# Kernel tuning notes

Hardware: AMD Instinct MI355X
Metric: run time of the kernel (lower is better)

## Reference

```python
import jax, jax.numpy as jnp
import numpy as np

H = 128        # hidden_dim
R = 50         # num_rbf
L = 4          # num_layers
CUTOFF = 5.0
N = 10000      # atoms
M = 64         # molecules
BOX = 54.7     # box side -> ~32 neighbors within cutoff
EPS = 1e-5     # LayerNorm eps (torch default)


def setup_inputs() -> dict:
    rng = np.random.default_rng(0)
    positions = rng.uniform(0.0, BOX, size=(N, 3)).astype(np.float32)
    # static radius graph (the torch module filters a dense NxN pair list by cutoff;
    # we do that once here so runtime shapes are fixed / jit-friendly)
    sq = (positions ** 2).sum(-1)
    d2 = sq[:, None] + sq[None, :] - 2.0 * positions @ positions.T
    mask = (d2 < CUTOFF * CUTOFF) & ~np.eye(N, dtype=bool)
    row, col = np.nonzero(mask)
    edge_index = jnp.asarray(np.stack([row, col]).astype(np.int32))  # [2, E]

    key = jax.random.key(0)
    ks = jax.random.split(key, 6)
    s = 0.05
    return dict(
        atomic_numbers=jax.random.randint(ks[0], (N,), 0, 100),
        positions=jnp.asarray(positions),
        batch=jnp.asarray((np.arange(N) * M // N).astype(np.int32)),  # sorted, all M present
        edge_index=edge_index,
        embedding=jax.random.normal(ks[1], (100, H), jnp.float32) * s,
        W1=jax.random.normal(ks[2], (L, H + R, H), jnp.float32) * s,
        b1=jnp.zeros((L, H), jnp.float32),
        W2=jax.random.normal(ks[3], (L, H, H), jnp.float32) * s,
        b2=jnp.zeros((L, H), jnp.float32),
        W_ih=jax.random.normal(ks[4], (L, H, 3 * H), jnp.float32) * s,
        b_ih=jax.random.normal(ks[5], (L, 3 * H), jnp.float32) * s,
        b_hh=jnp.zeros((L, 3 * H), jnp.float32),
        ln_g=jnp.ones((H,), jnp.float32),
        ln_b=jnp.zeros((H,), jnp.float32),
    )


def reference(atomic_numbers, positions, batch, edge_index, embedding,
              W1, b1, W2, b2, W_ih, b_ih, b_hh, ln_g, ln_b):
    x = embedding[jnp.clip(atomic_numbers, 0, 99)]                  # [N, H]
    row, col = edge_index[0], edge_index[1]
    d = jnp.linalg.norm(positions[row] - positions[col], axis=-1)   # [E]
    centers = jnp.linspace(0.0, CUTOFF, R)
    width = CUTOFF / R
    rbf = jnp.exp(-((d[:, None] - centers) ** 2) / (2.0 * width * width))  # [E, R]
    n_atoms = x.shape[0]
    for l in range(L):
        x_j = x[row]                                                # gather [E, H]
        inp = jnp.concatenate([x_j, rbf], axis=-1)                  # [E, H+R]
        msg = jax.nn.silu(inp @ W1[l] + b1[l]) @ W2[l] + b2[l]      # [E, H]
        aggr = jax.ops.segment_sum(msg, col, num_segments=n_atoms)  # [N, H]
        # GRU step with h0 = 0: W_hh @ h vanishes, only b_hh survives
        gi = aggr @ W_ih[l] + b_ih[l]                               # [N, 3H]
        gi_r, gi_z, gi_n = jnp.split(gi, 3, axis=-1)
        bh_r, bh_z, bh_n = jnp.split(b_hh[l], 3)
        r = jax.nn.sigmoid(gi_r + bh_r)
        z = jax.nn.sigmoid(gi_z + bh_z)
        n = jnp.tanh(gi_n + r * bh_n)
        x = x + (1.0 - z) * n                                       # h' = (1-z)*n + z*0
    mu = x.mean(-1, keepdims=True)
    var = ((x - mu) ** 2).mean(-1, keepdims=True)
    x = (x - mu) / jnp.sqrt(var + EPS) * ln_g + ln_b
    sums = jax.ops.segment_sum(x, batch, num_segments=M)            # [M, H]
    counts = jax.ops.segment_sum(jnp.ones((x.shape[0],), jnp.float32), batch, num_segments=M)
    graph_rep = sums / jnp.clip(counts, 1.0)[:, None]
    return x, graph_rep
```

## Files before the change

kernel.cpp:

```cpp
#include <hip/hip_runtime.h>
#include <hip/hip_bf16.h>
#include <math.h>


#define HH 128
#define RR 50
#define LL 4
#define GA 16
#define L2E 1.4426950408889634f

typedef __attribute__((ext_vector_type(8))) short short8;
typedef __attribute__((ext_vector_type(4))) float floatx4;

__device__ __forceinline__ unsigned short f2bf(float f) {
    unsigned u = __float_as_uint(f);
    unsigned r = (u + 0x7fffu + ((u >> 16) & 1u)) >> 16;
    return (unsigned short)r;
}
__device__ __forceinline__ unsigned pack_bf2(float lo, float hi) {
    unsigned u0 = __float_as_uint(lo) + 0x8000u;
    unsigned u1 = __float_as_uint(hi) + 0x8000u;
    return __builtin_amdgcn_perm(u1, u0, 0x07060302);
}
__device__ __forceinline__ float fast_sigmoid(float x) {
    return __builtin_amdgcn_rcpf(1.f + __builtin_amdgcn_exp2f(x * (-L2E)));
}
__device__ __forceinline__ float fast_tanh(float x) {
    x = fminf(fmaxf(x, -15.f), 15.f);
    float t = __builtin_amdgcn_exp2f(x * (2.f * L2E));
    return (t - 1.f) * __builtin_amdgcn_rcpf(t + 1.f);
}
__device__ __forceinline__ int imin(int a, int b) { return a < b ? a : b; }

__global__ __launch_bounds__(256) void prep_kernel(
    const int* __restrict__ an, const float* __restrict__ emb,
    float* __restrict__ X,
    const float* __restrict__ pos, const int* __restrict__ erow,
    const int* __restrict__ ecol, float* __restrict__ dist,
    int* __restrict__ rowptr, int* __restrict__ bptr,
    const int* __restrict__ batch,
    const float* __restrict__ W1, unsigned short* __restrict__ W1rT,
    unsigned short* __restrict__ W1xT,
    const float* __restrict__ W2, const float* __restrict__ Wih,
    unsigned short* __restrict__ WcT,
    const float* __restrict__ b2, float* __restrict__ P,
    const float* __restrict__ b1, unsigned short* __restrict__ embWbf,
    int* __restrict__ zc, float* __restrict__ outg,
    int N, int E, int M)
{
    int gidx = blockIdx.x * 256 + threadIdx.x;
    int c0 = N * HH;
    if (gidx < c0) {
        int i = gidx >> 7, n = gidx & 127;
        int z = an[i];
        z = z < 0 ? 0 : (z > 99 ? 99 : z);
        X[gidx] = emb[z * HH + n];
        return;
    }
    gidx -= c0;
    int PT = E > N ? E : N;
    if (gidx < PT) {
        int i = gidx;
        if (i < E) {
            int rc = erow[i];
            int rp = (i > 0) ? erow[i - 1] : -1;
            for (int r = rp + 1; r <= rc; ++r) rowptr[r] = i;
            if (i == E - 1)
                for (int r = rc + 1; r <= N; ++r) rowptr[r] = E;
        }
        if (i < N) {
            int bc = batch[i];
            int bp = (i > 0) ? batch[i - 1] : -1;
            for (int m = bp + 1; m <= bc; ++m) bptr[m] = i;
            if (i == N - 1)
                for (int m = bc + 1; m <= M; ++m) bptr[m] = N;
        }
        return;
    }
    gidx -= PT;
    if (gidx < E) {
        int e = gidx;
        int r = erow[e], c = ecol[e];
        float dx = pos[r * 3 + 0] - pos[c * 3 + 0];
        float dy = pos[r * 3 + 1] - pos[c * 3 + 1];
        float dz = pos[r * 3 + 2] - pos[c * 3 + 2];
        dist[e] = sqrtf(dx * dx + dy * dy + dz * dz);
        return;
    }
    gidx -= E;
    if (gidx < LL * HH * 64) {
        int l = gidx >> 13, rem = gidx & 8191;
        int f = rem >> 9, lane2 = (rem >> 3) & 63, j = rem & 7;
        int nt = f >> 1, h = f & 1;
        int n = nt * 16 + (lane2 & 15);
        int k = h * 32 + (lane2 >> 4) * 8 + j;
        float v = (k < RR) ? W1[((size_t)l * 178 + 128 + k) * HH + n] : 0.f;
        W1rT[gidx] = f2bf(v);
        return;
    }
    gidx -= LL * HH * 64;
    if (gidx < LL * HH * HH) {
        int l = gidx >> 14, rem = gidx & 16383, n = rem >> 7, k = rem & 127;
        W1xT[gidx] = f2bf(W1[((size_t)l * 178 + k) * HH + n]);
        return;
    }
    gidx -= LL * HH * HH;
    if (gidx < LL * HH * 384) {
        int l = gidx / (HH * 384), rem = gidx % (HH * 384);
        int i = rem / 384, j = rem % 384;
        const float* w2row = W2 + ((size_t)l * HH + i) * HH;
        const float* wih = Wih + (size_t)l * HH * 384;
        float acc = 0.f;
#pragma unroll 4
        for (int k = 0; k < HH; ++k)
            acc = fmaf(w2row[k], wih[(size_t)k * 384 + j], acc);
        WcT[((size_t)l * 384 + j) * HH + i] = f2bf(acc);
        return;
    }
    gidx -= LL * HH * 384;
    if (gidx < LL * 384) {
        int l = gidx / 384, j = gidx % 384;
        const float* b2l = b2 + (size_t)l * HH;
        const float* wih = Wih + (size_t)l * HH * 384;
        float acc = 0.f;
#pragma unroll 4
        for (int k = 0; k < HH; ++k)
            acc = fmaf(b2l[k], wih[(size_t)k * 384 + j], acc);
        P[gidx] = acc;
        return;
    }
    gidx -= LL * 384;
    if (gidx < N) {
        int z = an[gidx];
        zc[gidx] = z < 0 ? 0 : (z > 99 ? 99 : z);
        return;
    }
    gidx -= N;
    if (gidx < 100 * HH) {
        int z = gidx >> 7, n = gidx & 127;
        const float* er = emb + (size_t)z * HH;
        float acc = b1[n];
#pragma unroll 4
        for (int k = 0; k < HH; ++k)
            acc = fmaf(er[k], W1[(size_t)k * HH + n], acc);
        embWbf[gidx] = f2bf(acc);
        return;
    }
    gidx -= 100 * HH;
    if (gidx < M * HH) {
        outg[gidx] = 0.f;
    }
}

__global__ __launch_bounds__(256) void layer_kernel(
    const unsigned short* __restrict__ Xsrc, const unsigned short* __restrict__ W1rTf,
    const float* __restrict__ dist, const int* __restrict__ rowptr,
    const int* __restrict__ ecol, const int* __restrict__ zc, int use_z,
    const unsigned short* __restrict__ WcT, const float* __restrict__ P,
    const float* __restrict__ bih, const float* __restrict__ bhh,
    float* __restrict__ X, int N,
    const unsigned short* __restrict__ W1xT, const float* __restrict__ b1next,
    unsigned short* __restrict__ XWout, int do_xw,
    int do_ln, const float* __restrict__ lng, const float* __restrict__ lnb,
    const int* __restrict__ batch, const int* __restrict__ bptr,
    float* __restrict__ outx, float* __restrict__ outg)
{
    __shared__ __align__(16) unsigned short W1s[8192];
    __shared__ __align__(16) union ShMem {
        struct { unsigned short Sb[GA][136]; unsigned short Xb[GA][136]; } s;
        struct { float Xf[GA][132]; float pool[2][HH]; } f;
    } sh;
    unsigned short (&Sb)[GA][136] = sh.s.Sb;
    unsigned short (&Xb)[GA][136] = sh.s.Xb;
    float (&Xf)[GA][132] = sh.f.Xf;
    float (&pool)[2][HH] = sh.f.pool;

    int tid = threadIdx.x;
    {
        const uint4* src = (const uint4*)W1rTf;
        uint4* dst = (uint4*)W1s;
#pragma unroll
        for (int i = 0; i < 4; ++i) dst[tid + i * 256] = src[tid + i * 256];
    }
    __syncthreads();

    int abase = blockIdx.x * GA;
    int wavei = tid >> 6, lane = tid & 63;
    int c = lane & 15, q = lane >> 4;

    const float stepc = 5.0f / 49.0f;
    const float negc = -50.f * L2E;
    float kqs = (float)(q << 3) * stepc;

#pragma unroll 1
    for (int uu = wavei; uu < 2 * GA; uu += 4) {
        int a_loc = uu >> 1, h = uu & 1;
        int a = abase + a_loc;
        int es = 0, ee = 0;
        if (a < N) { es = rowptr[a]; ee = rowptr[a + 1]; }
        float acc[4][4];
#pragma unroll
        for (int t = 0; t < 4; ++t)
#pragma unroll
            for (int r = 0; r < 4; ++r) acc[t][r] = 0.f;

        if (es < ee) {
            int last = ee - 1;
            int ce0 = imin(es + c, last);
            float dcur = dist[ce0];
            int c0raw = ecol[ce0];
            int rowcur = use_z ? zc[c0raw] : c0raw;
            int ce1 = imin(es + 16 + c, last);
            float dnxt = dist[ce1];
            int colnxt = ecol[ce1];

            for (int eb = es; eb < ee; eb += 16) {
                const unsigned short* xwrow = Xsrc + (size_t)rowcur * HH + h * 64;
                uint2 gx[4];
#pragma unroll
                for (int t = 0; t < 4; ++t)
                    gx[t] = *(const uint2*)&xwrow[t * 16 + (q << 2)];

                float d_t = dcur;
                dcur = dnxt;
                int rownxt = use_z ? zc[colnxt] : colnxt;
                int ce2 = imin(eb + 32 + c, last);
                dnxt = dist[ce2];
                colnxt = ecol[ce2];
                rowcur = rownxt;

                float dq0 = d_t - kqs;
                float dq1 = dq0 - 32.f * stepc;
                union { unsigned u[4]; short8 s; } ub0, ub1;
#pragma unroll
                for (int p = 0; p < 4; ++p) {
                    float t0 = dq0 - (float)(2 * p) * stepc;
                    float t1 = dq0 - (float)(2 * p + 1) * stepc;
                    float e0f = __builtin_amdgcn_exp2f(negc * t0 * t0);
                    float e1f = __builtin_amdgcn_exp2f(negc * t1 * t1);
                    ub0.u[p] = pack_bf2(e0f, e1f);
                    float t2 = dq1 - (float)(2 * p) * stepc;
                    float t3 = dq1 - (float)(2 * p + 1) * stepc;
                    float e2f = __builtin_amdgcn_exp2f(negc * t2 * t2);
                    float e3f = __builtin_amdgcn_exp2f(negc * t3 * t3);
                    ub1.u[p] = pack_bf2(e2f, e3f);
                }
                short8 B0 = ub0.s, B1 = ub1.s;
                float msk = ((eb + c) < ee) ? 1.f : 0.f;

                unsigned wbyte = (unsigned)(lane * 16);
                asm volatile("" : "+v"(wbyte));
                const char* Wlp = (const char*)W1s + wbyte;

#pragma unroll
                for (int t = 0; t < 4; ++t) {
                    int f0 = (h * 4 + t) * 2;
                    short8 A0 = *(const short8*)(Wlp + f0 * 1024);
                    short8 A1 = *(const short8*)(Wlp + (f0 + 1) * 1024);
                    floatx4 C;
                    C[0] = __uint_as_float(gx[t].x << 16);
                    C[1] = __uint_as_float(gx[t].x & 0xffff0000u);
                    C[2] = __uint_as_float(gx[t].y << 16);
                    C[3] = __uint_as_float(gx[t].y & 0xffff0000u);
                    C = __builtin_amdgcn_mfma_f32_16x16x32_bf16(A0, B0, C, 0, 0, 0);
                    C = __builtin_amdgcn_mfma_f32_16x16x32_bf16(A1, B1, C, 0, 0, 0);
#pragma unroll
                    for (int r = 0; r < 4; ++r) {
                        float hh2 = C[r];
                        float v = hh2 * fast_sigmoid(hh2);
                        acc[t][r] = fmaf(v, msk, acc[t][r]);
                    }
                }
            }
        }

        int b0 = c & 1, b1 = (c >> 1) & 1, b2 = (c >> 2) & 1, b3 = (c >> 3) & 1;
        float s1[4][2];
#pragma unroll
        for (int t = 0; t < 4; ++t)
#pragma unroll
            for (int p = 0; p < 2; ++p) {
                float keep = b0 ? acc[t][2 * p + 1] : acc[t][2 * p];
                float send = b0 ? acc[t][2 * p] : acc[t][2 * p + 1];
                s1[t][p] = keep + __shfl_xor(send, 1, 64);
            }
        float s2[4];
#pragma unroll
        for (int t = 0; t < 4; ++t) {
            float keep = b1 ? s1[t][1] : s1[t][0];
            float send = b1 ? s1[t][0] : s1[t][1];
            s2[t] = keep + __shfl_xor(send, 2, 64);
        }
        float s3[2];
#pragma unroll
        for (int u2 = 0; u2 < 2; ++u2) {
            float keep = b2 ? s2[2 * u2 + 1] : s2[2 * u2];
            float send = b2 ? s2[2 * u2] : s2[2 * u2 + 1];
            s3[u2] = keep + __shfl_xor(send, 4, 64);
        }
        float keep = b3 ? s3[1] : s3[0];
        float send = b3 ? s3[0] : s3[1];
        float fin = keep + __shfl_xor(send, 8, 64);

        int t_fin = 2 * b3 + b2;
        int r_fin = 2 * b1 + b0;
        int n = t_fin * 16 + (q << 2) + r_fin;
        Sb[a_loc][h * 64 + n] = f2bf(fin);
    }
    __syncthreads();

    int wq = wavei;
    float pn[2][3], bi[2][3], bh[2][3], deg[4];
#pragma unroll
    for (int t = 0; t < 2; ++t) {
        int n = wq * 32 + t * 16 + c;
#pragma unroll
        for (int g = 0; g < 3; ++g) {
            pn[t][g] = P[g * 128 + n];
            bi[t][g] = bih[g * 128 + n];
            bh[t][g] = bhh[g * 128 + n];
        }
    }
#pragma unroll
    for (int r = 0; r < 4; ++r) {
        int a = abase + q * 4 + r;
        deg[r] = (a < N) ? (float)(rowptr[a + 1] - rowptr[a]) : 0.f;
    }

    floatx4 Cg[3][2];
#pragma unroll
    for (int g = 0; g < 3; ++g)
#pragma unroll
        for (int t = 0; t < 2; ++t)
            Cg[g][t] = floatx4{0.f, 0.f, 0.f, 0.f};

#pragma unroll
    for (int kt = 0; kt < 4; ++kt) {
        short8 A0 = *(const short8*)&Sb[c][kt * 32 + q * 8];
#pragma unroll
        for (int g = 0; g < 3; ++g)
#pragma unroll
            for (int t = 0; t < 2; ++t) {
                int nrow = g * 128 + wq * 32 + t * 16 + c;
                short8 B = *(const short8*)&WcT[(size_t)nrow * HH + kt * 32 + q * 8];
                Cg[g][t] = __builtin_amdgcn_mfma_f32_16x16x32_bf16(A0, B, Cg[g][t], 0, 0, 0);
            }
    }

    if (do_ln) __syncthreads();

#pragma unroll
    for (int r = 0; r < 4; ++r) {
        int am = q * 4 + r;
        int a = abase + am;
        bool ok = a < N;
#pragma unroll
        for (int t = 0; t < 2; ++t) {
            int n = wq * 32 + t * 16 + c;
            float g0 = Cg[0][t][r] + deg[r] * pn[t][0] + bi[t][0];
            float g1 = Cg[1][t][r] + deg[r] * pn[t][1] + bi[t][1];
            float g2 = Cg[2][t][r] + deg[r] * pn[t][2] + bi[t][2];
            float rr = fast_sigmoid(g0 + bh[t][0]);
            float zz = fast_sigmoid(g1 + bh[t][1]);
            float nn = fast_tanh(g2 + rr * bh[t][2]);
            float xv = 0.f;
            if (ok) {
                xv = X[(size_t)a * HH + n] + (1.f - zz) * nn;
                if (!do_ln) X[(size_t)a * HH + n] = xv;
            }
            if (do_ln) Xf[am][n] = xv;
            else       Xb[am][n] = f2bf(xv);
        }
    }

    if (do_ln) {
        (&pool[0][0])[tid] = 0.f;
        __syncthreads();

        int row = tid >> 4, j = tid & 15;
        int a2 = abase + row;
        float4 x0 = *(const float4*)&Xf[row][j * 8];
        float4 x1 = *(const float4*)&Xf[row][j * 8 + 4];
        float s = x0.x + x0.y + x0.z + x0.w + x1.x + x1.y + x1.z + x1.w;
        s += __shfl_xor(s, 1, 64);
        s += __shfl_xor(s, 2, 64);
        s += __shfl_xor(s, 4, 64);
        s += __shfl_xor(s, 8, 64);
        float mu = s * (1.f / 128.f);
        float qv = 0.f;
#define QACC(v) { float dx=(v).x-mu, dy=(v).y-mu, dz=(v).z-mu, dw=(v).w-mu; \
                  qv += dx*dx + dy*dy + dz*dz + dw*dw; }
        QACC(x0) QACC(x1)
#undef QACC
        qv += __shfl_xor(qv, 1, 64);
        qv += __shfl_xor(qv, 2, 64);
        qv += __shfl_xor(qv, 4, 64);
        qv += __shfl_xor(qv, 8, 64);
        float inv = rsqrtf(qv * (1.f / 128.f) + 1e-5f);

        int m0 = batch[abase];
        if (a2 < N) {
            int midx = batch[a2] - m0;
            const float4* gg = (const float4*)&lng[j * 8];
            const float4* bb = (const float4*)&lnb[j * 8];
            float* outrow = outx + (size_t)a2 * HH + j * 8;
            float* pl = &pool[midx][j * 8];
            float4 xs[2] = {x0, x1};
#pragma unroll
            for (int i = 0; i < 2; ++i) {
                float4 gv = gg[i], bv = bb[i], xv4 = xs[i];
                float4 y;
                y.x = (xv4.x - mu) * inv * gv.x + bv.x;
                y.y = (xv4.y - mu) * inv * gv.y + bv.y;
                y.z = (xv4.z - mu) * inv * gv.z + bv.z;
                y.w = (xv4.w - mu) * inv * gv.w + bv.w;
                *(float4*)(outrow + i * 4) = y;
                atomicAdd(pl + i * 4 + 0, y.x);
                atomicAdd(pl + i * 4 + 1, y.y);
                atomicAdd(pl + i * 4 + 2, y.z);
                atomicAdd(pl + i * 4 + 3, y.w);
            }
        }
        __syncthreads();

        int a_last = abase + GA - 1; if (a_last >= N) a_last = N - 1;
        int mlast = batch[a_last];
        int mi = tid >> 7, col = tid & 127;
        int m = m0 + mi;
        if (m <= mlast) {
            float cnt = (float)(bptr[m + 1] - bptr[m]);
            float invc = 1.f / fmaxf(cnt, 1.f);
            atomicAdd(&outg[(size_t)m * HH + col], pool[mi][col] * invc);
        }
        return;
    }

    if (!do_xw) return;
    __syncthreads();

    floatx4 Cx[2];
#pragma unroll
    for (int t = 0; t < 2; ++t)
        Cx[t] = floatx4{0.f, 0.f, 0.f, 0.f};
#pragma unroll
    for (int kt = 0; kt < 4; ++kt) {
        short8 A0 = *(const short8*)&Xb[c][kt * 32 + q * 8];
#pragma unroll
        for (int t = 0; t < 2; ++t) {
            int nrow = wq * 32 + t * 16 + c;
            short8 B = *(const short8*)&W1xT[(size_t)nrow * HH + kt * 32 + q * 8];
            Cx[t] = __builtin_amdgcn_mfma_f32_16x16x32_bf16(A0, B, Cx[t], 0, 0, 0);
        }
    }
#pragma unroll
    for (int r = 0; r < 4; ++r) {
        int a = abase + q * 4 + r;
        if (a >= N) continue;
#pragma unroll
        for (int t = 0; t < 2; ++t) {
            int n = wq * 32 + t * 16 + c;
            XWout[(size_t)a * HH + n] = f2bf(Cx[t][r] + b1next[n]);
        }
    }
}

extern "C" void kernel_launch(void* const* d_in, const int* in_sizes, int n_in,
                              void* d_out, int out_size, void* d_ws, size_t ws_size,
                              hipStream_t stream)
{
    const int*   an   = (const int*)d_in[0];
    const float* pos  = (const float*)d_in[1];
    const int*   bat  = (const int*)d_in[2];
    const int*   eidx = (const int*)d_in[3];
    const float* emb  = (const float*)d_in[4];
    const float* W1   = (const float*)d_in[5];
    const float* b1   = (const float*)d_in[6];
    const float* W2   = (const float*)d_in[7];
    const float* b2   = (const float*)d_in[8];
    const float* Wih  = (const float*)d_in[9];
    const float* bih  = (const float*)d_in[10];
    const float* bhh  = (const float*)d_in[11];
    const float* lng  = (const float*)d_in[12];
    const float* lnb  = (const float*)d_in[13];

    int N = in_sizes[0];
    int E = in_sizes[3] / 2;
    int M = out_size / HH - N;
    const int* erow = eidx;
    const int* ecol = eidx + E;

    float* ws   = (float*)d_ws;
    size_t off = 0;
    float* X    = ws + off; off += (size_t)N * HH;
    unsigned short* XWb0 = (unsigned short*)(ws + off); off += (size_t)N * HH / 2;
    unsigned short* XWb1 = (unsigned short*)(ws + off); off += (size_t)N * HH / 2;
    float* P    = ws + off; off += LL * 384;
    float* dist = ws + off; off += E;
    int* rowptr = (int*)(ws + off); off += N + 1;
    int* bptr   = (int*)(ws + off); off += M + 1;
    off = (off + 3) & ~(size_t)3;
    unsigned short* W1rT = (unsigned short*)(ws + off); off += (size_t)LL * HH * 32;
    unsigned short* W1xT = (unsigned short*)(ws + off); off += (size_t)LL * HH * 64;
    unsigned short* WcT  = (unsigned short*)(ws + off); off += (size_t)LL * 384 * 64;
    unsigned short* embWbf = (unsigned short*)(ws + off); off += (size_t)100 * HH / 2;
    int* zc     = (int*)(ws + off); off += N;

    float* outx = (float*)d_out;
    float* outg = outx + (size_t)N * HH;

    int PT = (E > N ? E : N);
    long total = (long)N * HH + PT + E + LL * HH * 64 + LL * HH * HH
               + LL * HH * 384 + LL * 384 + N + 100 * HH + (long)M * HH;
    int prep_blocks = (int)((total + 255) / 256);

    prep_kernel<<<prep_blocks, 256, 0, stream>>>(
        an, emb, X, pos, erow, ecol, dist, rowptr, bptr, bat,
        W1, W1rT, W1xT, W2, Wih, WcT, b2, P,
        b1, embWbf, zc, outg, N, E, M);

    int nb = (N + GA - 1) / GA;
    unsigned short* xwbuf[2] = {XWb0, XWb1};
    for (int l = 0; l < LL; ++l) {
        const unsigned short* src = (l == 0) ? embWbf : xwbuf[(l + 1) & 1];
        unsigned short* dst = xwbuf[l & 1];
        int do_xw = (l < LL - 1) ? 1 : 0;
        int do_ln = (l == LL - 1) ? 1 : 0;
        int ln = (l + 1 < LL) ? l + 1 : l;
        layer_kernel<<<nb, 256, 0, stream>>>(
            src, W1rT + (size_t)l * HH * 64, dist, rowptr, ecol, zc,
            (l == 0) ? 1 : 0,
            WcT + (size_t)l * 384 * HH, P + l * 384,
            bih + l * 384, bhh + l * 384, X, N,
            W1xT + (size_t)ln * HH * HH, b1 + (size_t)ln * HH, dst, do_xw,
            do_ln, lng, lnb, bat, bptr, outx, outg);
    }
}
```

Before: 327.7 us.

## Precompute bf16 RBF table once and split layer into edge and GRU kernels

The RBF expansion is now computed once in the prep kernel and stored as a bf16 [E,64] table, instead of being recomputed from distances with exp2 in every layer. Each layer's fused kernel is split into an edge-MFMA kernel, one wave per (atom, half), which writes aggregated messages to a global buffer, and a separate GRU/XW kernel that reads them back. This removes repeated transcendental work and gives the edge phase its own launch geometry. The cost is 128 extra bytes read per edge per layer, a global round trip for the aggregate, and twice as many kernel launches.

```diff
diff --git a/kernel.cpp b/kernel.cpp
--- a/kernel.cpp
+++ b/kernel.cpp
@@ -17,11 +17,6 @@
     unsigned r = (u + 0x7fffu + ((u >> 16) & 1u)) >> 16;
     return (unsigned short)r;
 }
-__device__ __forceinline__ unsigned pack_bf2(float lo, float hi) {
-    unsigned u0 = __float_as_uint(lo) + 0x8000u;
-    unsigned u1 = __float_as_uint(hi) + 0x8000u;
-    return __builtin_amdgcn_perm(u1, u0, 0x07060302);
-}
 __device__ __forceinline__ float fast_sigmoid(float x) {
     return __builtin_amdgcn_rcpf(1.f + __builtin_amdgcn_exp2f(x * (-L2E)));
 }
@@ -36,7 +31,7 @@
     const int* __restrict__ an, const float* __restrict__ emb,
     float* __restrict__ X,
     const float* __restrict__ pos, const int* __restrict__ erow,
-    const int* __restrict__ ecol, float* __restrict__ dist,
+    const int* __restrict__ ecol, unsigned short* __restrict__ rbfb,
     int* __restrict__ rowptr, int* __restrict__ bptr,
     const int* __restrict__ batch,
     const float* __restrict__ W1, unsigned short* __restrict__ W1rT,
@@ -78,16 +73,22 @@
         return;
     }
     gidx -= PT;
-    if (gidx < E) {
-        int e = gidx;
+    long rbfTot = (long)E * 64;
+    if (gidx < rbfTot) {
+        int e = gidx >> 6, k = gidx & 63;
         int r = erow[e], c = ecol[e];
         float dx = pos[r * 3 + 0] - pos[c * 3 + 0];
         float dy = pos[r * 3 + 1] - pos[c * 3 + 1];
         float dz = pos[r * 3 + 2] - pos[c * 3 + 2];
-        dist[e] = sqrtf(dx * dx + dy * dy + dz * dz);
-        return;
-    }
-    gidx -= E;
+        float d = sqrtf(dx * dx + dy * dy + dz * dz);
+        const float stepc = 5.0f / 49.0f;
+        const float negc = -50.f * L2E;
+        float t = d - (float)k * stepc;
+        float v = (k < RR) ? __builtin_amdgcn_exp2f(negc * t * t) : 0.f;
+        rbfb[gidx] = f2bf(v);
+        return;
+    }
+    gidx -= (int)rbfTot;
     if (gidx < LL * HH * 64) {
         int l = gidx >> 13, rem = gidx & 8191;
         int f = rem >> 9, lane2 = (rem >> 3) & 63, j = rem & 7;
@@ -152,29 +153,13 @@
     }
 }
 
-__global__ __launch_bounds__(256) void layer_kernel(
+__global__ __launch_bounds__(256) void edge_mfma_kernel(
     const unsigned short* __restrict__ Xsrc, const unsigned short* __restrict__ W1rTf,
-    const float* __restrict__ dist, const int* __restrict__ rowptr,
+    const unsigned short* __restrict__ rbfb, const int* __restrict__ rowptr,
     const int* __restrict__ ecol, const int* __restrict__ zc, int use_z,
-    const unsigned short* __restrict__ WcT, const float* __restrict__ P,
-    const float* __restrict__ bih, const float* __restrict__ bhh,
-    float* __restrict__ X, int N,
-    const unsigned short* __restrict__ W1xT, const float* __restrict__ b1next,
-    unsigned short* __restrict__ XWout, int do_xw,
-    int do_ln, const float* __restrict__ lng, const float* __restrict__ lnb,
-    const int* __restrict__ batch, const int* __restrict__ bptr,
-    float* __restrict__ outx, float* __restrict__ outg)
+    unsigned short* __restrict__ Sbf, int N, int nwaves)
 {
     __shared__ __align__(16) unsigned short W1s[8192];
-    __shared__ __align__(16) union ShMem {
-        struct { unsigned short Sb[GA][136]; unsigned short Xb[GA][136]; } s;
-        struct { float Xf[GA][132]; float pool[2][HH]; } f;
-    } sh;
-    unsigned short (&Sb)[GA][136] = sh.s.Sb;
-    unsigned short (&Xb)[GA][136] = sh.s.Xb;
-    float (&Xf)[GA][132] = sh.f.Xf;
-    float (&pool)[2][HH] = sh.f.pool;
-
     int tid = threadIdx.x;
     {
         const uint4* src = (const uint4*)W1rTf;
@@ -184,20 +169,14 @@
     }
     __syncthreads();
 
-    int abase = blockIdx.x * GA;
-    int wavei = tid >> 6, lane = tid & 63;
+    int wid = (blockIdx.x << 2) + (tid >> 6);
+    int lane = tid & 63;
     int c = lane & 15, q = lane >> 4;
 
-    const float stepc = 5.0f / 49.0f;
-    const float negc = -50.f * L2E;
-    float kqs = (float)(q << 3) * stepc;
-
-#pragma unroll 1
-    for (int uu = wavei; uu < 2 * GA; uu += 4) {
-        int a_loc = uu >> 1, h = uu & 1;
-        int a = abase + a_loc;
-        int es = 0, ee = 0;
-        if (a < N) { es = rowptr[a]; ee = rowptr[a + 1]; }
+    int NW = 2 * N;
+    for (int w = wid; w < NW; w += nwaves) {
+        int a = w >> 1, h = w & 1;
+        int es = rowptr[a], ee = rowptr[a + 1];
         float acc[4][4];
 #pragma unroll
         for (int t = 0; t < 4; ++t)
@@ -207,45 +186,28 @@
         if (es < ee) {
             int last = ee - 1;
             int ce0 = imin(es + c, last);
-            float dcur = dist[ce0];
             int c0raw = ecol[ce0];
             int rowcur = use_z ? zc[c0raw] : c0raw;
             int ce1 = imin(es + 16 + c, last);
-            float dnxt = dist[ce1];
             int colnxt = ecol[ce1];
 
             for (int eb = es; eb < ee; eb += 16) {
+                int ce = imin(eb + c, last);
+                const unsigned short* brow = rbfb + ((size_t)ce << 6) + (q << 3);
+                short8 B0 = *(const short8*)brow;
+                short8 B1 = *(const short8*)(brow + 32);
+
                 const unsigned short* xwrow = Xsrc + (size_t)rowcur * HH + h * 64;
                 uint2 gx[4];
 #pragma unroll
                 for (int t = 0; t < 4; ++t)
                     gx[t] = *(const uint2*)&xwrow[t * 16 + (q << 2)];
 
-                float d_t = dcur;
-                dcur = dnxt;
                 int rownxt = use_z ? zc[colnxt] : colnxt;
                 int ce2 = imin(eb + 32 + c, last);
-                dnxt = dist[ce2];
                 colnxt = ecol[ce2];
                 rowcur = rownxt;
 
-                float dq0 = d_t - kqs;
-                float dq1 = dq0 - 32.f * stepc;
-                union { unsigned u[4]; short8 s; } ub0, ub1;
-#pragma unroll
-                for (int p = 0; p < 4; ++p) {
-                    float t0 = dq0 - (float)(2 * p) * stepc;
-                    float t1 = dq0 - (float)(2 * p + 1) * stepc;
-                    float e0f = __builtin_amdgcn_exp2f(negc * t0 * t0);
-                    float e1f = __builtin_amdgcn_exp2f(negc * t1 * t1);
-                    ub0.u[p] = pack_bf2(e0f, e1f);
-                    float t2 = dq1 - (float)(2 * p) * stepc;
-                    float t3 = dq1 - (float)(2 * p + 1) * stepc;
-                    float e2f = __builtin_amdgcn_exp2f(negc * t2 * t2);
-                    float e3f = __builtin_amdgcn_exp2f(negc * t3 * t3);
-                    ub1.u[p] = pack_bf2(e2f, e3f);
-                }
-                short8 B0 = ub0.s, B1 = ub1.s;
                 float msk = ((eb + c) < ee) ? 1.f : 0.f;
 
                 unsigned wbyte = (unsigned)(lane * 16);
@@ -305,11 +267,34 @@
         int t_fin = 2 * b3 + b2;
         int r_fin = 2 * b1 + b0;
         int n = t_fin * 16 + (q << 2) + r_fin;
-        Sb[a_loc][h * 64 + n] = f2bf(fin);
-    }
-    __syncthreads();
-
-    int wq = wavei;
+        Sbf[(size_t)a * HH + h * 64 + n] = f2bf(fin);
+    }
+}
+
+__global__ __launch_bounds__(256) void grux_mfma_kernel(
+    const unsigned short* __restrict__ Sbf, const unsigned short* __restrict__ WcT,
+    const float* __restrict__ P, const float* __restrict__ bih,
+    const float* __restrict__ bhh, const int* __restrict__ rowptr,
+    float* __restrict__ X, int N,
+    const unsigned short* __restrict__ W1xT, const float* __restrict__ b1next,
+    unsigned short* __restrict__ XWout, int do_xw,
+    int do_ln, const float* __restrict__ lng, const float* __restrict__ lnb,
+    const int* __restrict__ batch, const int* __restrict__ bptr,
+    float* __restrict__ outx, float* __restrict__ outg)
+{
+    __shared__ __align__(16) union ShMem {
+        struct { unsigned short Sb[GA][136]; unsigned short Xb[GA][136]; } s;
+        struct { float Xf[GA][132]; float pool[2][HH]; } f;
+    } sh;
+    unsigned short (&Sb)[GA][136] = sh.s.Sb;
+    unsigned short (&Xb)[GA][136] = sh.s.Xb;
+    float (&Xf)[GA][132] = sh.f.Xf;
+    float (&pool)[2][HH] = sh.f.pool;
+
+    int tid = threadIdx.x;
+    int abase = blockIdx.x * GA;
+    int wq = tid >> 6, lane = tid & 63, c = lane & 15, q = lane >> 4;
+
     float pn[2][3], bi[2][3], bh[2][3], deg[4];
 #pragma unroll
     for (int t = 0; t < 2; ++t) {
@@ -326,6 +311,14 @@
         int a = abase + q * 4 + r;
         deg[r] = (a < N) ? (float)(rowptr[a + 1] - rowptr[a]) : 0.f;
     }
+
+    {
+        int a = tid >> 4, ch = tid & 15;
+        int aa = abase + a; if (aa >= N) aa = N - 1;
+        uint4 v = *(const uint4*)(Sbf + (size_t)aa * HH + ch * 8);
+        *(uint4*)&Sb[a][ch * 8] = v;
+    }
+    __syncthreads();
 
     floatx4 Cg[3][2];
 #pragma unroll
@@ -492,13 +485,13 @@
     float* ws   = (float*)d_ws;
     size_t off = 0;
     float* X    = ws + off; off += (size_t)N * HH;
-    unsigned short* XWb0 = (unsigned short*)(ws + off); off += (size_t)N * HH / 2;
-    unsigned short* XWb1 = (unsigned short*)(ws + off); off += (size_t)N * HH / 2;
+    unsigned short* Sbf = (unsigned short*)(ws + off); off += (size_t)N * HH / 2;
+    unsigned short* XWb = (unsigned short*)(ws + off); off += (size_t)N * HH / 2;
     float* P    = ws + off; off += LL * 384;
-    float* dist = ws + off; off += E;
     int* rowptr = (int*)(ws + off); off += N + 1;
     int* bptr   = (int*)(ws + off); off += M + 1;
     off = (off + 3) & ~(size_t)3;
+    unsigned short* rbfb = (unsigned short*)(ws + off); off += (size_t)E * 32;
     unsigned short* W1rT = (unsigned short*)(ws + off); off += (size_t)LL * HH * 32;
     unsigned short* W1xT = (unsigned short*)(ws + off); off += (size_t)LL * HH * 64;
     unsigned short* WcT  = (unsigned short*)(ws + off); off += (size_t)LL * 384 * 64;
@@ -509,29 +502,29 @@
     float* outg = outx + (size_t)N * HH;
 
     int PT = (E > N ? E : N);
-    long total = (long)N * HH + PT + E + LL * HH * 64 + LL * HH * HH
+    long total = (long)N * HH + PT + (long)E * 64 + LL * HH * 64 + LL * HH * HH
                + LL * HH * 384 + LL * 384 + N + 100 * HH + (long)M * HH;
     int prep_blocks = (int)((total + 255) / 256);
 
     prep_kernel<<<prep_blocks, 256, 0, stream>>>(
-        an, emb, X, pos, erow, ecol, dist, rowptr, bptr, bat,
+        an, emb, X, pos, erow, ecol, rbfb, rowptr, bptr, bat,
         W1, W1rT, W1xT, W2, Wih, WcT, b2, P,
         b1, embWbf, zc, outg, N, E, M);
 
-    int nb = (N + GA - 1) / GA;
-    unsigned short* xwbuf[2] = {XWb0, XWb1};
+    int eblocks = (2 * N + 3) / 4;
+    int nwaves = eblocks * 4;
+    int grux_blocks = (N + GA - 1) / GA;
     for (int l = 0; l < LL; ++l) {
-        const unsigned short* src = (l == 0) ? embWbf : xwbuf[(l + 1) & 1];
-        unsigned short* dst = xwbuf[l & 1];
+        edge_mfma_kernel<<<eblocks, 256, 0, stream>>>(
+            (l == 0) ? embWbf : XWb, W1rT + (size_t)l * HH * 64,
+            rbfb, rowptr, ecol, zc, (l == 0) ? 1 : 0, Sbf, N, nwaves);
         int do_xw = (l < LL - 1) ? 1 : 0;
         int do_ln = (l == LL - 1) ? 1 : 0;
         int ln = (l + 1 < LL) ? l + 1 : l;
-        layer_kernel<<<nb, 256, 0, stream>>>(
-            src, W1rT + (size_t)l * HH * 64, dist, rowptr, ecol, zc,
-            (l == 0) ? 1 : 0,
-            WcT + (size_t)l * 384 * HH, P + l * 384,
-            bih + l * 384, bhh + l * 384, X, N,
-            W1xT + (size_t)ln * HH * HH, b1 + (size_t)ln * HH, dst, do_xw,
+        grux_mfma_kernel<<<grux_blocks, 256, 0, stream>>>(
+            Sbf, WcT + (size_t)l * 384 * HH, P + l * 384,
+            bih + l * 384, bhh + l * 384, rowptr, X, N,
+            W1xT + (size_t)ln * HH * HH, b1 + (size_t)ln * HH, XWb, do_xw,
             do_ln, lng, lnb, bat, bptr, outx, outg);
     }
 }
```

New measurement: 358.8 us. 1.09x slower.
